# Kernel optimization log

Hardware: AMD Instinct MI355X
Metric: run time of the kernel (lower is better)

Reference implementation:

```python
import jax, jax.numpy as jnp
import numpy as np

N_HEAD = 16

def setup_inputs() -> dict:
    key = jax.random.key(0)
    ks = jax.random.split(key, 9)
    H = 2048
    def w(k, shape, scale=0.02):
        return jax.random.normal(k, shape, dtype=jnp.float32) * scale
    return {
        'h':  jax.random.normal(ks[0], (4, 2048, H), dtype=jnp.float32),
        'Wq': w(ks[1], (H, H)), 'bq': w(ks[2], (H,)),
        'Wk': w(ks[3], (H, H)), 'bk': w(ks[4], (H,)),
        'Wv': w(ks[5], (H, H)), 'bv': w(ks[6], (H,)),
        'Wo': w(ks[7], (H, H)), 'bo': w(ks[8], (H,)),
    }

def reference(h, Wq, bq, Wk, bk, Wv, bv, Wo, bo):
    B, S, H = h.shape
    nh = N_HEAD
    hd = H // nh
    # QKV projections (torch Linear: x @ W.T + b)
    q = (h @ Wq.T + bq).reshape(B, S, nh, hd)
    k = (h @ Wk.T + bk).reshape(B, S, nh, hd)
    v = (h @ Wv.T + bv).reshape(B, S, nh, hd)
    scale = 1.0 / jnp.sqrt(jnp.float32(hd))
    # causal attention scores [B, nh, S, S]
    scores = jnp.einsum('bqhd,bkhd->bhqk', q, k) * scale
    causal = jnp.tril(jnp.ones((S, S), dtype=bool))
    scores = jnp.where(causal, scores, jnp.finfo(scores.dtype).min)
    attn = jax.nn.softmax(scores, axis=-1)
    o = jnp.einsum('bhqk,bkhd->bqhd', attn, v).reshape(B, S, H)
    return o @ Wo.T + bo
```

## Files before the change

### kernel.cpp

```cpp
#include <hip/hip_runtime.h>
#include <hip/hip_bf16.h>
#include <math.h>


using bf16x8 = __attribute__((ext_vector_type(8))) __bf16;
using f32x4  = __attribute__((ext_vector_type(4))) float;
using s16x8  = __attribute__((ext_vector_type(8))) short;

#define MFMA16(a, b, c) __builtin_amdgcn_mfma_f32_16x16x32_bf16((a), (b), (c), 0, 0, 0)

__device__ __forceinline__ unsigned short f2bf(float f) {
  unsigned u = __float_as_uint(f);
  u += 0x7FFFu + ((u >> 16) & 1u);
  return (unsigned short)(u >> 16);
}

__device__ __forceinline__ void gload16(const void* g, void* l) {
  __builtin_amdgcn_global_load_lds((const __attribute__((address_space(1))) void*)g,
                                   (__attribute__((address_space(3))) void*)l,
                                   16, 0, 0);
}

__global__ void cvt_kernel(const float* __restrict__ in, unsigned short* __restrict__ out, int n4) {
  int i = blockIdx.x * 256 + threadIdx.x;
  if (i >= n4) return;
  float4 v = ((const float4*)in)[i];
  ushort4 o;
  o.x = f2bf(v.x); o.y = f2bf(v.y); o.z = f2bf(v.z); o.w = f2bf(v.w);
  ((ushort4*)out)[i] = o;
}


#define GEMM_PRE()                                                             \
  const int tid = threadIdx.x;                                                 \
  const int wave = tid >> 6, lane = tid & 63;                                  \
  const int lo = lane & 15, hi = lane >> 4;                                    \
  const int wr = wave >> 2, wc = wave & 3;                                     \
  const int r4 = lane >> 2, s4 = lane & 3;                                     \
  const int scol = ((s4 ^ ((r4 >> 1) & 3)) << 3);                              \
  const unsigned short* aS[2]; const unsigned short* bS[2];                    \
  _Pragma("unroll")                                                            \
  for (int j = 0; j < 2; ++j) {                                                \
    aS[j] = A + (size_t)(m0 + (wave * 2 + j) * 16 + r4) * 2048 + scol;         \
    bS[j] = W + (size_t)(n0 + (wave * 2 + j) * 16 + r4) * 2048 + scol;         \
  }                                                                            \
  f32x4 acc[8][4] = {};

#define STAGE2(BUF, J)                                                         \
  do {                                                                         \
    gload16(aS[J], &lA[BUF][(wave * 2 + (J)) * 512]);                          \
    gload16(bS[J], &lB[BUF][(wave * 2 + (J)) * 512]);                          \
    aS[J] += 32; bS[J] += 32;                                                  \
  } while (0)

#define LDA4_(dst, MH, BUF)                                                    \
  do {                                                                         \
    _Pragma("unroll")                                                          \
    for (int im = 0; im < 4; ++im)                                             \
      dst[im] = *(const bf16x8*)&lA[BUF][(wr * 128 + (MH)*64 + im * 16 + lo) * 32 + \
                                         ((hi ^ ((lo >> 1) & 3)) << 3)];       \
  } while (0)

#define LDB4_(dst, BUF)                                                        \
  do {                                                                         \
    _Pragma("unroll")                                                          \
    for (int ni = 0; ni < 4; ++ni)                                             \
      dst[ni] = *(const bf16x8*)&lB[BUF][(wc * 64 + ni * 16 + lo) * 32 +       \
                                         ((hi ^ ((lo >> 1) & 3)) << 3)];       \
  } while (0)

#define MF16(MH, aF, bF)                                                       \
  do {                                                                         \
    __builtin_amdgcn_s_setprio(1);                                             \
    _Pragma("unroll")                                                          \
    for (int im = 0; im < 4; ++im)                                             \
      _Pragma("unroll")                                                        \
      for (int ni = 0; ni < 4; ++ni)                                           \
        acc[(MH)*4 + im][ni] = MFMA16(aF[im], bF[ni], acc[(MH)*4 + im][ni]);   \
    __builtin_amdgcn_s_setprio(0);                                             \
  } while (0)

#define BAR __builtin_amdgcn_s_barrier()
#define VMC(N) asm volatile("s_waitcnt vmcnt(" #N ")" ::: "memory")

#define TILE(RBUF, SBUF, COND, VN)                                             \
  do {                                                                         \
    bf16x8 aF[4], aG[4], bF[4];                                                \
    LDA4_(aF, 0, RBUF); LDB4_(bF, RBUF);                                       \
    if (COND) { STAGE2(SBUF, 0); STAGE2(SBUF, 1); }                            \
    BAR;                                                                       \
    MF16(0, aF, bF);                                                           \
    LDA4_(aG, 1, RBUF);                                                        \
    MF16(1, aG, bF);                                                           \
    VMC(VN); BAR;                                                              \
  } while (0)

#define GEMM_MAIN()                                                            \
  STAGE2(0, 0); STAGE2(0, 1); STAGE2(1, 0); STAGE2(1, 1);                      \
  STAGE2(2, 0); STAGE2(2, 1);                                                  \
  VMC(8); BAR;                                                                 \
  for (int u = 0; u < 15; ++u) {                                               \
    TILE(0, 3, true, 8); TILE(1, 0, true, 8);                                  \
    TILE(2, 1, true, 8); TILE(3, 2, true, 8);                                  \
  }                                                                            \
  TILE(0, 3, true, 8); TILE(1, 0, false, 4);                                   \
  TILE(2, 1, false, 0); TILE(3, 2, false, 0);

__global__ __launch_bounds__(512, 2)
void gemm_qkv(const unsigned short* __restrict__ A,
              const unsigned short* __restrict__ W,
              const float* __restrict__ bq, const float* __restrict__ bk,
              const float* __restrict__ bv,
              unsigned short* __restrict__ Q, unsigned short* __restrict__ Kq,
              unsigned short* __restrict__ V) {
  __shared__ unsigned short lA[4][256 * 32];
  __shared__ unsigned short lB[4][256 * 32];
  const int bid = blockIdx.x;
  const int sid = (bid & 7) * 96 + (bid >> 3);
  const int bm = sid / 24, bn = sid % 24;
  const int m0 = bm * 256, n0 = bn * 256;
  GEMM_PRE();
  GEMM_MAIN();

  const int which = n0 >> 11;
  const float* bias = (which == 0) ? bq : (which == 1) ? bk : bv;
  unsigned short* dst = (which == 0) ? Q : (which == 1) ? Kq : V;
#pragma unroll
  for (int mi = 0; mi < 8; mi++)
#pragma unroll
    for (int ni = 0; ni < 4; ni++) {
      int n_g = n0 + wc * 64 + ni * 16 + lo;
      int n2 = n_g & 2047;
      int head = n2 >> 7, d = n2 & 127;
      float bb = bias[n2];
#pragma unroll
      for (int i = 0; i < 4; i++) {
        int m = m0 + wr * 128 + mi * 16 + hi * 4 + i;
        int b = m >> 11, s = m & 2047;
        dst[(((size_t)b * 16 + head) * 2048 + s) * 128 + d] = f2bf(acc[mi][ni][i] + bb);
      }
    }
}

__global__ __launch_bounds__(512, 2)
void gemm_out(const unsigned short* __restrict__ A,
              const unsigned short* __restrict__ W,
              const float* __restrict__ bo, float* __restrict__ out) {
  __shared__ unsigned short lA[4][256 * 32];
  __shared__ unsigned short lB[4][256 * 32];
  const int bid = blockIdx.x;
  const int sid = (bid & 7) * 32 + (bid >> 3);
  const int bm = sid >> 3, bn = sid & 7;
  const int m0 = bm * 256, n0 = bn * 256;
  GEMM_PRE();
  GEMM_MAIN();

#pragma unroll
  for (int mi = 0; mi < 8; mi++)
#pragma unroll
    for (int ni = 0; ni < 4; ni++) {
      int n_g = n0 + wc * 64 + ni * 16 + lo;
      float bb = bo[n_g];
#pragma unroll
      for (int i = 0; i < 4; i++) {
        int m = m0 + wr * 128 + mi * 16 + hi * 4 + i;
        out[(size_t)m * 2048 + n_g] = acc[mi][ni][i] + bb;
      }
    }
}

__global__ __launch_bounds__(256, 2)
void attn_kernel(const unsigned short* __restrict__ Qb,
                 const unsigned short* __restrict__ Kb,
                 const unsigned short* __restrict__ Vb,
                 unsigned short* __restrict__ Ob) {
  __shared__ unsigned short lK[64 * 128];
  __shared__ unsigned short lVt[144 * 72];
  __shared__ unsigned short lP[4][32 * 72];

  const int tid = threadIdx.x;
  const int wave = tid >> 6, lane = tid & 63;
  const int lo = lane & 15, hi = lane >> 4;
  const int bh = blockIdx.x & 63;
  const int qt = 15 - (blockIdx.x >> 6);
  const int q0 = qt * 128 + wave * 32;
  const size_t base = (size_t)bh * 2048 * 128;
  const float SCL = 0.08838834764831845f * 1.4426950408889634f;
  const float THR = 11.5416f;

#pragma unroll
  for (int x = tid; x < 1024; x += 256)
    lVt[(128 + (x >> 6)) * 72 + (x & 63)] = 0x3F80;

  bf16x8 aq[2][4];
#pragma unroll
  for (int mi = 0; mi < 2; mi++)
#pragma unroll
    for (int dk = 0; dk < 4; dk++)
      aq[mi][dk] = *(const bf16x8*)&Qb[base + (size_t)(q0 + mi * 16 + lo) * 128 + dk * 32 + hi * 8];

  f32x4 acc[2][9] = {};
  float mrun[2][4];
#pragma unroll
  for (int a = 0; a < 2; a++)
#pragma unroll
    for (int b = 0; b < 4; b++) mrun[a][b] = -INFINITY;

  const int ktn = qt * 2 + 2;
  const int qmax_w = q0 + 31;

  for (int kt = 0; kt < ktn; kt++) {
    __syncthreads();
#pragma unroll
    for (int j = 0; j < 4; j++) {
      int lrow = j * 16 + wave * 4 + hi;
      int srccol = (lo * 16) ^ ((lrow & 7) << 4);
      gload16(Kb + base + (size_t)(kt * 64 + lrow) * 128 + (srccol >> 1),
              &lK[(j * 16 + wave * 4) * 128]);
    }
    {
      int rr = tid & 31;
      int c0 = (tid >> 5) * 8;
#pragma unroll
      for (int half = 0; half < 2; half++) {
        int cc = c0 + half * 64;
        const unsigned short* vp = Vb + base + (size_t)(kt * 64 + 2 * rr) * 128 + cc;
        s16x8 va = *(const s16x8*)vp;
        s16x8 vb2 = *(const s16x8*)(vp + 128);
#pragma unroll
        for (int j = 0; j < 8; j++)
          *(ushort2*)&lVt[(cc + j) * 72 + 2 * rr] =
              make_ushort2((unsigned short)va[j], (unsigned short)vb2[j]);
      }
    }
    __syncthreads();

    if (kt * 64 <= qmax_w) {
      f32x4 sc[2][4] = {};
#pragma unroll
      for (int ni = 0; ni < 4; ni++)
#pragma unroll
        for (int dk = 0; dk < 4; dk++) {
          int row = ni * 16 + lo;
          int col = (dk * 32 + hi * 8) ^ ((row & 7) << 3);
          bf16x8 bk_ = *(const bf16x8*)&lK[row * 128 + col];
          sc[0][ni] = MFMA16(aq[0][dk], bk_, sc[0][ni]);
          sc[1][ni] = MFMA16(aq[1][dk], bk_, sc[1][ni]);
        }

      float tm[2][4];
      bool cond = true;
#pragma unroll
      for (int mi = 0; mi < 2; mi++)
#pragma unroll
        for (int i = 0; i < 4; i++) {
          int qrow = q0 + mi * 16 + hi * 4 + i;
          float mx = -INFINITY;
#pragma unroll
          for (int ni = 0; ni < 4; ni++) {
            int kc = kt * 64 + ni * 16 + lo;
            float s = sc[mi][ni][i] * SCL;
            if (kc > qrow) s = -INFINITY;
            sc[mi][ni][i] = s;
            mx = fmaxf(mx, s);
          }
          tm[mi][i] = mx;
          cond = cond && (mx <= mrun[mi][i] + THR);
        }

      if (!__all((int)cond)) {
#pragma unroll
        for (int mi = 0; mi < 2; mi++)
#pragma unroll
          for (int i = 0; i < 4; i++) {
            float mt = tm[mi][i];
            mt = fmaxf(mt, __shfl_xor(mt, 1));
            mt = fmaxf(mt, __shfl_xor(mt, 2));
            mt = fmaxf(mt, __shfl_xor(mt, 4));
            mt = fmaxf(mt, __shfl_xor(mt, 8));
            float mo = mrun[mi][i];
            float mn = fmaxf(mo, mt);
            float alpha = exp2f(mo - mn);
            mrun[mi][i] = mn;
#pragma unroll
            for (int ni = 0; ni < 9; ni++) acc[mi][ni][i] *= alpha;
          }
      }

      unsigned short* lPw = &lP[wave][0];
#pragma unroll
      for (int mi = 0; mi < 2; mi++)
#pragma unroll
        for (int i = 0; i < 4; i++) {
          float m = mrun[mi][i];
          int prow = mi * 16 + hi * 4 + i;
#pragma unroll
          for (int ni = 0; ni < 4; ni++)
            lPw[prow * 72 + ni * 16 + lo] = f2bf(exp2f(sc[mi][ni][i] - m));
        }

      bf16x8 ap[2][2];
#pragma unroll
      for (int mi = 0; mi < 2; mi++)
#pragma unroll
        for (int k2 = 0; k2 < 2; k2++)
          ap[mi][k2] = *(const bf16x8*)&lPw[(mi * 16 + lo) * 72 + k2 * 32 + hi * 8];
#pragma unroll
      for (int ni = 0; ni < 9; ni++)
#pragma unroll
        for (int k2 = 0; k2 < 2; k2++) {
          bf16x8 bv_ = *(const bf16x8*)&lVt[(ni * 16 + lo) * 72 + k2 * 32 + hi * 8];
          acc[0][ni] = MFMA16(ap[0][k2], bv_, acc[0][ni]);
          acc[1][ni] = MFMA16(ap[1][k2], bv_, acc[1][ni]);
        }
    }
  }

  const int b = bh >> 4, hh = bh & 15;
#pragma unroll
  for (int mi = 0; mi < 2; mi++)
#pragma unroll
    for (int i = 0; i < 4; i++) {
      float inv = 1.0f / acc[mi][8][i];
      int s = q0 + mi * 16 + hi * 4 + i;
      size_t rowbase = ((size_t)b * 2048 + s) * 2048 + hh * 128 + lo;
#pragma unroll
      for (int ni = 0; ni < 8; ni++)
        Ob[rowbase + ni * 16] = f2bf(acc[mi][ni][i] * inv);
    }
}

extern "C" void kernel_launch(void* const* d_in, const int* in_sizes, int n_in,
                              void* d_out, int out_size, void* d_ws, size_t ws_size,
                              hipStream_t stream) {
  const float* h  = (const float*)d_in[0];
  const float* Wq = (const float*)d_in[1];
  const float* bq = (const float*)d_in[2];
  const float* Wk = (const float*)d_in[3];
  const float* bk = (const float*)d_in[4];
  const float* Wv = (const float*)d_in[5];
  const float* bv = (const float*)d_in[6];
  const float* Wo = (const float*)d_in[7];
  const float* bo = (const float*)d_in[8];
  float* out = (float*)d_out;

  char* ws = (char*)d_ws;
  unsigned short* h_bf  = (unsigned short*)(ws + 0);
  unsigned short* Qb    = (unsigned short*)(ws + 33554432);
  unsigned short* Kb    = (unsigned short*)(ws + 67108864);
  unsigned short* Vb    = (unsigned short*)(ws + 100663296);
  unsigned short* Wqkv  = (unsigned short*)(ws + 134217728);
  unsigned short* Wo_bf = (unsigned short*)(ws + 159383552);
  unsigned short* Ob    = h_bf;

  cvt_kernel<<<16384, 256, 0, stream>>>(h, h_bf, 4194304);
  cvt_kernel<<<4096, 256, 0, stream>>>(Wq, Wqkv, 1048576);
  cvt_kernel<<<4096, 256, 0, stream>>>(Wk, Wqkv + 4194304, 1048576);
  cvt_kernel<<<4096, 256, 0, stream>>>(Wv, Wqkv + 8388608, 1048576);
  cvt_kernel<<<4096, 256, 0, stream>>>(Wo, Wo_bf, 1048576);

  gemm_qkv<<<dim3(768), dim3(512), 0, stream>>>(h_bf, Wqkv, bq, bk, bv, Qb, Kb, Vb);

  attn_kernel<<<dim3(1024), dim3(256), 0, stream>>>(Qb, Kb, Vb, Ob);

  gemm_out<<<dim3(256), dim3(512), 0, stream>>>(Ob, Wo_bf, bo, out);
}
```

Measured before the change: 455.1 us.

## Restructure GEMM K-pipeline, double-buffer attention K tiles, merge weight conversions

```diff
diff --git a/kernel.cpp b/kernel.cpp
--- a/kernel.cpp
+++ b/kernel.cpp
@@ -30,6 +30,20 @@
   ((ushort4*)out)[i] = o;
 }
 
+__global__ void cvtW_kernel(const float* __restrict__ s0, const float* __restrict__ s1,
+                            const float* __restrict__ s2, const float* __restrict__ s3,
+                            unsigned short* __restrict__ dqkv, unsigned short* __restrict__ dwo) {
+  int i = blockIdx.x * 256 + threadIdx.x;
+  int which = i >> 20;
+  const float* s = (which == 0) ? s0 : (which == 1) ? s1 : (which == 2) ? s2 : s3;
+  unsigned short* d = (which < 3) ? dqkv + which * 4194304 : dwo;
+  int j = i & 1048575;
+  float4 v = ((const float4*)s)[j];
+  ushort4 o;
+  o.x = f2bf(v.x); o.y = f2bf(v.y); o.z = f2bf(v.z); o.w = f2bf(v.w);
+  ((ushort4*)d)[j] = o;
+}
+
 
 #define GEMM_PRE()                                                             \
   const int tid = threadIdx.x;                                                 \
@@ -38,35 +52,42 @@
   const int wr = wave >> 2, wc = wave & 3;                                     \
   const int r4 = lane >> 2, s4 = lane & 3;                                     \
   const int scol = ((s4 ^ ((r4 >> 1) & 3)) << 3);                              \
-  const unsigned short* aS[2]; const unsigned short* bS[2];                    \
+  const unsigned short* aBase[2]; const unsigned short* bBase[2];              \
   _Pragma("unroll")                                                            \
   for (int j = 0; j < 2; ++j) {                                                \
-    aS[j] = A + (size_t)(m0 + (wave * 2 + j) * 16 + r4) * 2048 + scol;         \
-    bS[j] = W + (size_t)(n0 + (wave * 2 + j) * 16 + r4) * 2048 + scol;         \
+    aBase[j] = A + (size_t)(m0 + (wave * 2 + j) * 16 + r4) * 2048 + scol;      \
+    bBase[j] = W + (size_t)(n0 + (wave * 2 + j) * 16 + r4) * 2048 + scol;      \
   }                                                                            \
   f32x4 acc[8][4] = {};
 
-#define STAGE2(BUF, J)                                                         \
-  do {                                                                         \
-    gload16(aS[J], &lA[BUF][(wave * 2 + (J)) * 512]);                          \
-    gload16(bS[J], &lB[BUF][(wave * 2 + (J)) * 512]);                          \
-    aS[J] += 32; bS[J] += 32;                                                  \
-  } while (0)
-
-#define LDA4_(dst, MH, BUF)                                                    \
+#define STAGEA(BUF, KH, KOFF)                                                  \
+  do {                                                                         \
+    _Pragma("unroll")                                                          \
+    for (int j = 0; j < 2; ++j)                                                \
+      gload16(aBase[j] + (KOFF), &lA[BUF][KH][(wave * 2 + j) * 512]);          \
+  } while (0)
+
+#define STAGEB(BUF, KH, KOFF)                                                  \
+  do {                                                                         \
+    _Pragma("unroll")                                                          \
+    for (int j = 0; j < 2; ++j)                                                \
+      gload16(bBase[j] + (KOFF), &lB[BUF][KH][(wave * 2 + j) * 512]);          \
+  } while (0)
+
+#define LDA4_(dst, MH, BUF, KH)                                                \
   do {                                                                         \
     _Pragma("unroll")                                                          \
     for (int im = 0; im < 4; ++im)                                             \
-      dst[im] = *(const bf16x8*)&lA[BUF][(wr * 128 + (MH)*64 + im * 16 + lo) * 32 + \
-                                         ((hi ^ ((lo >> 1) & 3)) << 3)];       \
-  } while (0)
-
-#define LDB4_(dst, BUF)                                                        \
+      dst[im] = *(const bf16x8*)&lA[BUF][KH][(wr * 128 + (MH)*64 + im * 16 + lo) * 32 + \
+                                             ((hi ^ ((lo >> 1) & 3)) << 3)];   \
+  } while (0)
+
+#define LDB4_(dst, BUF, KH)                                                    \
   do {                                                                         \
     _Pragma("unroll")                                                          \
     for (int ni = 0; ni < 4; ++ni)                                             \
-      dst[ni] = *(const bf16x8*)&lB[BUF][(wc * 64 + ni * 16 + lo) * 32 +       \
-                                         ((hi ^ ((lo >> 1) & 3)) << 3)];       \
+      dst[ni] = *(const bf16x8*)&lB[BUF][KH][(wc * 64 + ni * 16 + lo) * 32 +   \
+                                             ((hi ^ ((lo >> 1) & 3)) << 3)];   \
   } while (0)
 
 #define MF16(MH, aF, bF)                                                       \
@@ -83,28 +104,37 @@
 #define BAR __builtin_amdgcn_s_barrier()
 #define VMC(N) asm volatile("s_waitcnt vmcnt(" #N ")" ::: "memory")
 
-#define TILE(RBUF, SBUF, COND, VN)                                             \
+#define TILE64(B, BX, C1, C2, VN)                                              \
   do {                                                                         \
     bf16x8 aF[4], aG[4], bF[4];                                                \
-    LDA4_(aF, 0, RBUF); LDB4_(bF, RBUF);                                       \
-    if (COND) { STAGE2(SBUF, 0); STAGE2(SBUF, 1); }                            \
-    BAR;                                                                       \
-    MF16(0, aF, bF);                                                           \
-    LDA4_(aG, 1, RBUF);                                                        \
-    MF16(1, aG, bF);                                                           \
-    VMC(VN); BAR;                                                              \
+    LDA4_(aF, 0, B, 0); LDB4_(bF, B, 0);                                       \
+    if (C1) STAGEA(BX, 1, kbase + 96);                                         \
+    BAR; MF16(0, aF, bF); BAR;                                                 \
+    LDA4_(aG, 1, B, 0);                                                        \
+    if (C1) STAGEB(BX, 1, kbase + 96);                                         \
+    BAR; MF16(1, aG, bF); BAR;                                                 \
+    LDA4_(aF, 0, B, 1); LDB4_(bF, B, 1);                                       \
+    if (C2) STAGEA(B, 0, kbase + 128);                                         \
+    BAR; MF16(0, aF, bF); BAR;                                                 \
+    LDA4_(aG, 1, B, 1);                                                        \
+    if (C2) STAGEB(B, 0, kbase + 128);                                         \
+    BAR; MF16(1, aG, bF); VMC(VN); BAR;                                        \
+    kbase += 64;                                                               \
   } while (0)
 
 #define GEMM_MAIN()                                                            \
-  STAGE2(0, 0); STAGE2(0, 1); STAGE2(1, 0); STAGE2(1, 1);                      \
-  STAGE2(2, 0); STAGE2(2, 1);                                                  \
-  VMC(8); BAR;                                                                 \
-  for (int u = 0; u < 15; ++u) {                                               \
-    TILE(0, 3, true, 8); TILE(1, 0, true, 8);                                  \
-    TILE(2, 1, true, 8); TILE(3, 2, true, 8);                                  \
+  int kbase = 0;                                                               \
+  STAGEA(0, 0, 0); STAGEB(0, 0, 0);                                            \
+  STAGEA(0, 1, 32); STAGEB(0, 1, 32);                                          \
+  STAGEA(1, 0, 64); STAGEB(1, 0, 64);                                          \
+  VMC(4); BAR;                                                                 \
+  for (int u = 0; u < 14; ++u) {                                               \
+    TILE64(0, 1, true, true, 4); TILE64(1, 0, true, true, 4);                  \
   }                                                                            \
-  TILE(0, 3, true, 8); TILE(1, 0, false, 4);                                   \
-  TILE(2, 1, false, 0); TILE(3, 2, false, 0);
+  TILE64(0, 1, true, true, 4);                                                 \
+  TILE64(1, 0, true, true, 4);                                                 \
+  TILE64(0, 1, true, false, 0);                                                \
+  TILE64(1, 0, false, false, 0);
 
 __global__ __launch_bounds__(512, 2)
 void gemm_qkv(const unsigned short* __restrict__ A,
@@ -113,8 +143,8 @@
               const float* __restrict__ bv,
               unsigned short* __restrict__ Q, unsigned short* __restrict__ Kq,
               unsigned short* __restrict__ V) {
-  __shared__ unsigned short lA[4][256 * 32];
-  __shared__ unsigned short lB[4][256 * 32];
+  __shared__ unsigned short lA[2][2][256 * 32];
+  __shared__ unsigned short lB[2][2][256 * 32];
   const int bid = blockIdx.x;
   const int sid = (bid & 7) * 96 + (bid >> 3);
   const int bm = sid / 24, bn = sid % 24;
@@ -146,8 +176,8 @@
 void gemm_out(const unsigned short* __restrict__ A,
               const unsigned short* __restrict__ W,
               const float* __restrict__ bo, float* __restrict__ out) {
-  __shared__ unsigned short lA[4][256 * 32];
-  __shared__ unsigned short lB[4][256 * 32];
+  __shared__ unsigned short lA[2][2][256 * 32];
+  __shared__ unsigned short lB[2][2][256 * 32];
   const int bid = blockIdx.x;
   const int sid = (bid & 7) * 32 + (bid >> 3);
   const int bm = sid >> 3, bn = sid & 7;
@@ -174,7 +204,7 @@
                  const unsigned short* __restrict__ Kb,
                  const unsigned short* __restrict__ Vb,
                  unsigned short* __restrict__ Ob) {
-  __shared__ unsigned short lK[64 * 128];
+  __shared__ unsigned short lK[2][64 * 128];
   __shared__ unsigned short lVt[144 * 72];
   __shared__ unsigned short lP[4][32 * 72];
 
@@ -208,34 +238,34 @@
 
   const int ktn = qt * 2 + 2;
   const int qmax_w = q0 + 31;
+  const int rr = tid & 31, c0v = (tid >> 5) * 8;
+
+#define STAGEK(KT2, BUF)                                                       \
+  do {                                                                         \
+    _Pragma("unroll")                                                          \
+    for (int j = 0; j < 4; j++) {                                              \
+      int lrow = j * 16 + wave * 4 + hi;                                       \
+      int srccol = (lo * 16) ^ ((lrow & 7) << 4);                              \
+      gload16(Kb + base + (size_t)((KT2) * 64 + lrow) * 128 + (srccol >> 1),   \
+              &lK[BUF][(j * 16 + wave * 4) * 128]);                            \
+    }                                                                          \
+  } while (0)
+
+  STAGEK(0, 0);
 
   for (int kt = 0; kt < ktn; kt++) {
-    __syncthreads();
-#pragma unroll
-    for (int j = 0; j < 4; j++) {
-      int lrow = j * 16 + wave * 4 + hi;
-      int srccol = (lo * 16) ^ ((lrow & 7) << 4);
-      gload16(Kb + base + (size_t)(kt * 64 + lrow) * 128 + (srccol >> 1),
-              &lK[(j * 16 + wave * 4) * 128]);
-    }
-    {
-      int rr = tid & 31;
-      int c0 = (tid >> 5) * 8;
-#pragma unroll
-      for (int half = 0; half < 2; half++) {
-        int cc = c0 + half * 64;
-        const unsigned short* vp = Vb + base + (size_t)(kt * 64 + 2 * rr) * 128 + cc;
-        s16x8 va = *(const s16x8*)vp;
-        s16x8 vb2 = *(const s16x8*)(vp + 128);
-#pragma unroll
-        for (int j = 0; j < 8; j++)
-          *(ushort2*)&lVt[(cc + j) * 72 + 2 * rr] =
-              make_ushort2((unsigned short)va[j], (unsigned short)vb2[j]);
-      }
-    }
-    __syncthreads();
-
-    if (kt * 64 <= qmax_w) {
+    const unsigned short* vp0 = Vb + base + (size_t)(kt * 64 + 2 * rr) * 128 + c0v;
+    s16x8 v00 = *(const s16x8*)vp0;
+    s16x8 v01 = *(const s16x8*)(vp0 + 128);
+    s16x8 v10 = *(const s16x8*)(vp0 + 64);
+    s16x8 v11 = *(const s16x8*)(vp0 + 192);
+    if (kt + 1 < ktn) { STAGEK(kt + 1, (kt + 1) & 1); VMC(8); }
+    else { VMC(4); }
+    BAR;
+
+    const bool docomp = (kt * 64 <= qmax_w);
+    if (docomp) {
+      const unsigned short* lKc = &lK[kt & 1][0];
       f32x4 sc[2][4] = {};
 #pragma unroll
       for (int ni = 0; ni < 4; ni++)
@@ -243,11 +273,10 @@
         for (int dk = 0; dk < 4; dk++) {
           int row = ni * 16 + lo;
           int col = (dk * 32 + hi * 8) ^ ((row & 7) << 3);
-          bf16x8 bk_ = *(const bf16x8*)&lK[row * 128 + col];
+          bf16x8 bk_ = *(const bf16x8*)&lKc[row * 128 + col];
           sc[0][ni] = MFMA16(aq[0][dk], bk_, sc[0][ni]);
           sc[1][ni] = MFMA16(aq[1][dk], bk_, sc[1][ni]);
         }
-
       float tm[2][4];
       bool cond = true;
 #pragma unroll
@@ -267,7 +296,6 @@
           tm[mi][i] = mx;
           cond = cond && (mx <= mrun[mi][i] + THR);
         }
-
       if (!__all((int)cond)) {
 #pragma unroll
         for (int mi = 0; mi < 2; mi++)
@@ -286,7 +314,6 @@
             for (int ni = 0; ni < 9; ni++) acc[mi][ni][i] *= alpha;
           }
       }
-
       unsigned short* lPw = &lP[wave][0];
 #pragma unroll
       for (int mi = 0; mi < 2; mi++)
@@ -298,7 +325,21 @@
           for (int ni = 0; ni < 4; ni++)
             lPw[prow * 72 + ni * 16 + lo] = f2bf(exp2f(sc[mi][ni][i] - m));
         }
-
+    }
+
+    if (kt + 1 < ktn) VMC(4); else VMC(0);
+#pragma unroll
+    for (int j = 0; j < 8; j++) {
+      *(ushort2*)&lVt[(c0v + j) * 72 + 2 * rr] =
+          make_ushort2((unsigned short)v00[j], (unsigned short)v01[j]);
+      *(ushort2*)&lVt[(c0v + 64 + j) * 72 + 2 * rr] =
+          make_ushort2((unsigned short)v10[j], (unsigned short)v11[j]);
+    }
+    asm volatile("s_waitcnt lgkmcnt(0)" ::: "memory");
+    BAR;
+
+    if (docomp) {
+      unsigned short* lPw = &lP[wave][0];
       bf16x8 ap[2][2];
 #pragma unroll
       for (int mi = 0; mi < 2; mi++)
@@ -354,10 +395,7 @@
   unsigned short* Ob    = h_bf;
 
   cvt_kernel<<<16384, 256, 0, stream>>>(h, h_bf, 4194304);
-  cvt_kernel<<<4096, 256, 0, stream>>>(Wq, Wqkv, 1048576);
-  cvt_kernel<<<4096, 256, 0, stream>>>(Wk, Wqkv + 4194304, 1048576);
-  cvt_kernel<<<4096, 256, 0, stream>>>(Wv, Wqkv + 8388608, 1048576);
-  cvt_kernel<<<4096, 256, 0, stream>>>(Wo, Wo_bf, 1048576);
+  cvtW_kernel<<<16384, 256, 0, stream>>>(Wq, Wk, Wv, Wo, Wqkv, Wo_bf);
 
   gemm_qkv<<<dim3(768), dim3(512), 0, stream>>>(h_bf, Wqkv, bq, bk, bv, Qb, Kb, Vb);
 
```

After: 450.6 us. About the same (-1.0%).
